# Kernel optimization log

Measured on AMD Instinct MI355X. Metric: run time of the kernel, lower is better.

## Reference

```python
import jax, jax.numpy as jnp
import numpy as np

FILTER_WIDTH = 23
NSIG = 9.0
RATIO = 4.0
SUB_LOW_RATIO = 1.0
PCT = 3.0  # normalization_percentile_threshold


def _gaussian_kernel_2d(ksize, sigma):
    # matches cv2.getGaussianKernel for sigma > 0: normalized 1D gaussian, outer product
    i = np.arange(ksize, dtype=np.float64) - (ksize - 1) / 2.0
    k1 = np.exp(-(i ** 2) / (2.0 * sigma ** 2))
    k1 /= k1.sum()
    k2 = np.outer(k1, k1)
    return k2.astype(np.float32)


def setup_inputs() -> dict:
    key = jax.random.key(0)
    k1, k2 = jax.random.split(key)
    x = jax.random.normal(k1, (16, 3, 512, 512), dtype=jnp.float32)
    mask = jax.random.uniform(k2, (16, 1, 512, 512), dtype=jnp.float32)
    kernel = jnp.asarray(_gaussian_kernel_2d(FILTER_WIDTH, NSIG))[None, None]  # [1,1,23,23]
    return {"x": x, "mask": mask, "kernel": kernel}


def reference(x, mask, kernel):
    N, C, H, W = x.shape
    pad = FILTER_WIDTH // 2  # 11

    # --- median padding (torch.median = lower median -> sorted index (n-1)//2) ---
    flat = x.reshape(N, C, H * W)
    med = jnp.sort(flat, axis=-1)[:, :, (H * W - 1) // 2] + 0.2  # [N,C]
    med = med[:, :, None, None]
    xp = mask * x + (1.0 - mask) * med  # [N,C,H,W]

    # --- Gaussian low-pass: replication pad + depthwise conv (same kernel per channel) ---
    xpad = jnp.pad(xp, ((0, 0), (0, 0), (pad, pad), (pad, pad)), mode="edge")
    k = jnp.broadcast_to(kernel, (C, 1, FILTER_WIDTH, FILTER_WIDTH))
    gauss = jax.lax.conv_general_dilated(
        xpad, k, window_strides=(1, 1), padding="VALID", feature_group_count=C
    )  # [N,C,H,W]

    res = RATIO * (xp - SUB_LOW_RATIO * gauss)

    # --- per-(n,c) percentile normalization on 1/256-quantized copy ---
    temp = jnp.trunc(res * 256.0) / 256.0  # torch .int() truncates toward zero
    tflat = temp.reshape(N, C, H * W)
    lo = jnp.percentile(tflat, PCT, axis=-1)[:, :, None, None]
    hi = jnp.percentile(tflat, 100.0 - PCT, axis=-1)[:, :, None, None]
    res = (res - lo) / (hi - lo)

    # sub_mask=True
    return res * mask
```

## Files before the change

### kernel.cpp

```cpp
#include <hip/hip_runtime.h>

#define HW 262144
#define WID 512
#define PLANES 48
#define NCH 3
#define PAD 11
#define FW 23
#define XS 92
#define NSUB 16

__device__ __forceinline__ float uniform_f(float v) {
  return __uint_as_float((unsigned)__builtin_amdgcn_readfirstlane((int)__float_as_uint(v)));
}

__global__ __launch_bounds__(256) void hist1_kernel(const float* __restrict__ x,
                                                    ushort* __restrict__ part) {
  __shared__ int h[8192];
  const int p = blockIdx.x, s = blockIdx.y, tid = threadIdx.x;
  for (int i = tid; i < 8192; i += 256) h[i] = 0;
  __syncthreads();
  const float4* xv = (const float4*)(x + (size_t)p * HW + (size_t)s * (HW / NSUB));
  float4 a[8], b[8];
#pragma unroll
  for (int q = 0; q < 8; ++q) a[q] = xv[tid + q * 256];
#pragma unroll
  for (int q = 0; q < 8; ++q) b[q] = xv[tid + (8 + q) * 256];
#define H1(c) { int bin = (int)(((c) + 8.0f) * 512.0f); bin = min(max(bin, 0), 8191); atomicAdd(&h[bin], 1); }
#pragma unroll
  for (int q = 0; q < 8; ++q) { H1(a[q].x); H1(a[q].y); H1(a[q].z); H1(a[q].w); }
#pragma unroll
  for (int q = 0; q < 8; ++q) { H1(b[q].x); H1(b[q].y); H1(b[q].z); H1(b[q].w); }
#undef H1
  __syncthreads();
  uint4* out = (uint4*)(part + ((size_t)p * NSUB + s) * 8192);
  for (int k = tid; k < 1024; k += 256) {
    int4 c = *(const int4*)&h[k * 8];
    int4 d = *(const int4*)&h[k * 8 + 4];
    uint4 w;
    w.x = (unsigned)c.x | ((unsigned)c.y << 16);
    w.y = (unsigned)c.z | ((unsigned)c.w << 16);
    w.z = (unsigned)d.x | ((unsigned)d.y << 16);
    w.w = (unsigned)d.z | ((unsigned)d.w << 16);
    out[k] = w;
  }
}

__global__ __launch_bounds__(256) void scan_med_kernel(const ushort* __restrict__ part,
                                                       float* __restrict__ med,
                                                       const float* __restrict__ kern,
                                                       float* __restrict__ k1g) {
  __shared__ int hsum[8192];
  __shared__ int incl[256];
  __shared__ int s_chunk, s_base;
  const int p = blockIdx.x, t = threadIdx.x;
  if (p == 0 && t < FW) k1g[t] = kern[t * FW + PAD] / sqrtf(kern[PAD * FW + PAD]);
  const uint4* pr = (const uint4*)(part + (size_t)p * NSUB * 8192);
  for (int idx = t; idx < 1024; idx += 256) {
    int a0=0,a1=0,a2=0,a3=0,a4=0,a5=0,a6=0,a7=0;
#pragma unroll
    for (int s = 0; s < NSUB; ++s) {
      uint4 v = pr[(size_t)s * 1024 + idx];
      a0 += (int)(v.x & 0xffff); a1 += (int)(v.x >> 16);
      a2 += (int)(v.y & 0xffff); a3 += (int)(v.y >> 16);
      a4 += (int)(v.z & 0xffff); a5 += (int)(v.z >> 16);
      a6 += (int)(v.w & 0xffff); a7 += (int)(v.w >> 16);
    }
    int* hb = &hsum[idx * 8];
    hb[0]=a0; hb[1]=a1; hb[2]=a2; hb[3]=a3; hb[4]=a4; hb[5]=a5; hb[6]=a6; hb[7]=a7;
  }
  __syncthreads();
  int mysum = 0;
#pragma unroll
  for (int j = 0; j < 32; j += 4) {
    int4 v = *(const int4*)&hsum[t * 32 + j];
    mysum += v.x + v.y + v.z + v.w;
  }
  incl[t] = mysum;
  __syncthreads();
  for (int off = 1; off < 256; off <<= 1) {
    int v = (t >= off) ? incl[t - off] : 0;
    __syncthreads();
    incl[t] += v;
    __syncthreads();
  }
  const int rank = 131072;
  {
    int excl = incl[t] - mysum;
    if (excl < rank && rank <= incl[t]) { s_chunk = t; s_base = rank - excl; }
  }
  __syncthreads();
  if (t < 64) {
    const int c = s_chunk, base = s_base;
    int cnt = (t < 32) ? hsum[c * 32 + t] : 0;
    int pfx = cnt;
#pragma unroll
    for (int off = 1; off < 32; off <<= 1) {
      int u = __shfl_up(pfx, off, 64);
      if (t >= off) pfx += u;
    }
    unsigned long long m = __ballot(t < 32 && pfx >= base);
    int bin = c * 32 + (__ffsll((long long)m) - 1);
    if (t == 0) med[p] = -8.0f + ((float)bin + 0.5f) * 0.001953125f + 0.2f;
  }
}

__global__ __launch_bounds__(256) void conv_kernel(const float* __restrict__ x,
                                                   const float* __restrict__ mask,
                                                   const float* __restrict__ k1g,
                                                   const float* __restrict__ med,
                                                   float* __restrict__ res) {
  __shared__ float xs[86 * XS];
  const int z = blockIdx.z;
  const int n = z / NCH;
  const int tbx = blockIdx.x, tby = blockIdx.y;
  const int tid = threadIdx.x;

  float k1[FW];
#pragma unroll
  for (int t = 0; t < FW; ++t) k1[t] = uniform_f(k1g[t]);

  const float m_med = uniform_f(med[z]);
  const int gr0 = tby * 64 - PAD;
  const int gc0 = tbx * 64 - PAD;
  const float* xb = x + (size_t)z * HW;
  const float* mb = mask + (size_t)n * HW;
  for (int i = tid; i < 86 * 86; i += 256) {
    int r = i / 86, c = i - r * 86;
    int gr = min(max(gr0 + r, 0), WID - 1);
    int gc = min(max(gc0 + c, 0), WID - 1);
    int g = gr * WID + gc;
    float xv = xb[g], mv = mb[g];
    xs[r * XS + c] = fmaf(mv, xv - m_med, m_med);
  }
  __syncthreads();

  float ah[3][8];
#pragma unroll
  for (int it = 0; it < 3; ++it) {
    const int g = tid + (it << 8);
    if (g < 86 * 8) {
      const int r = g >> 3, c0 = (g & 7) << 3;
      const float* row = &xs[r * XS + c0];
      float w[32];
#pragma unroll
      for (int q = 0; q < 8; ++q) *(float4*)&w[q * 4] = *(const float4*)(row + q * 4);
#pragma unroll
      for (int j = 0; j < 8; ++j) ah[it][j] = 0.f;
#pragma unroll
      for (int t = 0; t < FW; ++t) {
        const float k = k1[t];
#pragma unroll
        for (int j = 0; j < 8; ++j) ah[it][j] = fmaf(k, w[t + j], ah[it][j]);
      }
    }
  }

  const int ct = (tid & 15) << 2;
  const int rt = (tid >> 4) << 2;
  float4 xpA[4], xpB[4];
#pragma unroll
  for (int j = 0; j < 4; ++j) {
    const float* xr = &xs[(rt + j + PAD) * XS + ct];
    xpA[j] = *(const float4*)(xr + 8);
    xpB[j] = *(const float4*)(xr + 12);
  }
  __syncthreads();

#pragma unroll
  for (int it = 0; it < 3; ++it) {
    const int g = tid + (it << 8);
    if (g < 86 * 8) {
      const int r = g >> 3, c0 = (g & 7) << 3;
      *(float4*)&xs[r * XS + c0] = make_float4(ah[it][0], ah[it][1], ah[it][2], ah[it][3]);
      *(float4*)&xs[r * XS + c0 + 4] = make_float4(ah[it][4], ah[it][5], ah[it][6], ah[it][7]);
    }
  }
  __syncthreads();

  float4 acc[4];
#pragma unroll
  for (int j = 0; j < 4; ++j) acc[j] = make_float4(0.f, 0.f, 0.f, 0.f);
#pragma unroll
  for (int tp = 0; tp < 26; ++tp) {
    float4 v = *(const float4*)&xs[(rt + tp) * XS + ct];
    const int jlo = (tp - 22 > 0) ? (tp - 22) : 0;
    const int jhi = (tp < 3) ? tp : 3;
#pragma unroll
    for (int j = jlo; j <= jhi; ++j) {
      float k = k1[tp - j];
      acc[j].x = fmaf(k, v.x, acc[j].x);
      acc[j].y = fmaf(k, v.y, acc[j].y);
      acc[j].z = fmaf(k, v.z, acc[j].z);
      acc[j].w = fmaf(k, v.w, acc[j].w);
    }
  }

  float* rb = res + (size_t)z * HW + (size_t)(tby * 64 + rt) * WID + tbx * 64 + ct;
#pragma unroll
  for (int j = 0; j < 4; ++j) {
    float4 o;
    o.x = 4.0f * (xpA[j].w - acc[j].x);
    o.y = 4.0f * (xpB[j].x - acc[j].y);
    o.z = 4.0f * (xpB[j].y - acc[j].z);
    o.w = 4.0f * (xpB[j].z - acc[j].w);
    *(float4*)(rb + (size_t)j * WID) = o;
  }
}

__global__ __launch_bounds__(256) void hist_kernel(const float* __restrict__ res,
                                                   ushort* __restrict__ part) {
  __shared__ int h[8192];
  const int p = blockIdx.x, s = blockIdx.y, tid = threadIdx.x;
  for (int i = tid; i < 8192; i += 256) h[i] = 0;
  __syncthreads();
  const float4* rv = (const float4*)(res + (size_t)p * HW + (size_t)s * (HW / NSUB));
  float4 a[8], b[8];
#pragma unroll
  for (int q = 0; q < 8; ++q) a[q] = rv[tid + q * 256];
#pragma unroll
  for (int q = 0; q < 8; ++q) b[q] = rv[tid + (8 + q) * 256];
#define HADD(c) { int bin = (int)((c) * 256.0f) + 4096; bin = min(max(bin, 0), 8191); atomicAdd(&h[bin], 1); }
#pragma unroll
  for (int q = 0; q < 8; ++q) { HADD(a[q].x); HADD(a[q].y); HADD(a[q].z); HADD(a[q].w); }
#pragma unroll
  for (int q = 0; q < 8; ++q) { HADD(b[q].x); HADD(b[q].y); HADD(b[q].z); HADD(b[q].w); }
#undef HADD
  __syncthreads();
  uint4* out = (uint4*)(part + ((size_t)p * NSUB + s) * 8192);
  for (int k = tid; k < 1024; k += 256) {
    int4 c = *(const int4*)&h[k * 8];
    int4 d = *(const int4*)&h[k * 8 + 4];
    uint4 w;
    w.x = (unsigned)c.x | ((unsigned)c.y << 16);
    w.y = (unsigned)c.z | ((unsigned)c.w << 16);
    w.z = (unsigned)d.x | ((unsigned)d.y << 16);
    w.w = (unsigned)d.z | ((unsigned)d.w << 16);
    out[k] = w;
  }
}

__global__ __launch_bounds__(256) void pct_kernel(const ushort* __restrict__ part,
                                                  float* __restrict__ lo_out,
                                                  float* __restrict__ inv_out) {
  __shared__ int hsum[8192];
  __shared__ int incl[256];
  __shared__ int s_chunk, s_base;
  __shared__ float s_v[4];
  const int p = blockIdx.x, t = threadIdx.x;
  const uint4* pr = (const uint4*)(part + (size_t)p * NSUB * 8192);
  for (int idx = t; idx < 1024; idx += 256) {
    int a0=0,a1=0,a2=0,a3=0,a4=0,a5=0,a6=0,a7=0;
#pragma unroll
    for (int s = 0; s < NSUB; ++s) {
      uint4 v = pr[(size_t)s * 1024 + idx];
      a0 += (int)(v.x & 0xffff); a1 += (int)(v.x >> 16);
      a2 += (int)(v.y & 0xffff); a3 += (int)(v.y >> 16);
      a4 += (int)(v.z & 0xffff); a5 += (int)(v.z >> 16);
      a6 += (int)(v.w & 0xffff); a7 += (int)(v.w >> 16);
    }
    int* hb = &hsum[idx * 8];
    hb[0]=a0; hb[1]=a1; hb[2]=a2; hb[3]=a3; hb[4]=a4; hb[5]=a5; hb[6]=a6; hb[7]=a7;
  }
  __syncthreads();
  int mysum = 0;
#pragma unroll
  for (int j = 0; j < 32; j += 4) {
    int4 v = *(const int4*)&hsum[t * 32 + j];
    mysum += v.x + v.y + v.z + v.w;
  }
  incl[t] = mysum;
  __syncthreads();
  for (int off = 1; off < 256; off <<= 1) {
    int v = (t >= off) ? incl[t - off] : 0;
    __syncthreads();
    incl[t] += v;
    __syncthreads();
  }
  const int ranks[4] = {7865, 7866, 254279, 254280};
#pragma unroll
  for (int r = 0; r < 4; ++r) {
    const int rank = ranks[r];
    int excl = incl[t] - mysum;
    if (excl < rank && rank <= incl[t]) { s_chunk = t; s_base = rank - excl; }
    __syncthreads();
    if (t < 64) {
      const int c = s_chunk, base = s_base;
      int cnt = (t < 32) ? hsum[c * 32 + t] : 0;
      int pfx = cnt;
#pragma unroll
      for (int off = 1; off < 32; off <<= 1) {
        int u = __shfl_up(pfx, off, 64);
        if (t >= off) pfx += u;
      }
      unsigned long long m = __ballot(t < 32 && pfx >= base);
      int bin = c * 32 + (__ffsll((long long)m) - 1);
      if (t == 0) s_v[r] = (float)(bin - 4096) * 0.00390625f;
    }
    __syncthreads();
  }
  if (t == 0) {
    const double fl = 0.29, fh = 0.71;
    double lov = (double)s_v[0] + fl * ((double)s_v[1] - (double)s_v[0]);
    double hiv = (double)s_v[2] + fh * ((double)s_v[3] - (double)s_v[2]);
    lo_out[p] = (float)lov;
    inv_out[p] = (float)(1.0 / (hiv - lov));
  }
}

__global__ __launch_bounds__(256) void final_kernel(float* __restrict__ res,
                                                    const float* __restrict__ mask,
                                                    const float* __restrict__ lo,
                                                    const float* __restrict__ inv) {
  const int base = blockIdx.x * 512 + threadIdx.x;
  const int z = base >> 16;
  const int n = z / NCH;
  const int h0 = base & 65535;
  float4* rz = (float4*)res;
  const float4* mz = (const float4*)mask + (size_t)n * 65536;
  float4 r0 = rz[base], r1 = rz[base + 256];
  float4 m0 = mz[h0], m1 = mz[h0 + 256];
  const float l = lo[z];
  const float iv = inv[z];
  float4 o0, o1;
  o0.x = (r0.x - l) * iv * m0.x;  o0.y = (r0.y - l) * iv * m0.y;
  o0.z = (r0.z - l) * iv * m0.z;  o0.w = (r0.w - l) * iv * m0.w;
  o1.x = (r1.x - l) * iv * m1.x;  o1.y = (r1.y - l) * iv * m1.y;
  o1.z = (r1.z - l) * iv * m1.z;  o1.w = (r1.w - l) * iv * m1.w;
  rz[base] = o0;
  rz[base + 256] = o1;
}

extern "C" void kernel_launch(void* const* d_in, const int* in_sizes, int n_in,
                              void* d_out, int out_size, void* d_ws, size_t ws_size,
                              hipStream_t stream) {
  (void)in_sizes; (void)n_in; (void)out_size; (void)ws_size;
  const float* x = (const float*)d_in[0];
  const float* mask = (const float*)d_in[1];
  const float* kern = (const float*)d_in[2];
  float* out = (float*)d_out;

  ushort* part = (ushort*)d_ws;
  float* med = (float*)(part + (size_t)PLANES * NSUB * 8192);
  float* lo = med + PLANES;
  float* inv = lo + PLANES;
  float* k1g = inv + PLANES;

  hist1_kernel<<<dim3(PLANES, NSUB), 256, 0, stream>>>(x, part);
  scan_med_kernel<<<PLANES, 256, 0, stream>>>(part, med, kern, k1g);
  conv_kernel<<<dim3(8, 8, PLANES), 256, 0, stream>>>(x, mask, k1g, med, out);
  hist_kernel<<<dim3(PLANES, NSUB), 256, 0, stream>>>(out, part);
  pct_kernel<<<PLANES, 256, 0, stream>>>(part, lo, inv);
  final_kernel<<<(HW * PLANES / 8) / 256, 256, 0, stream>>>(out, mask, lo, inv);
}
```

Baseline: 194.1 us.

## Fuse histogram reduction into histogram kernels via last-block atomic ticket

The separate scan/median and percentile kernels are merged into the two histogram kernels. Each block bumps a per-plane atomic counter after writing its partial histogram, and the last block for that plane does the reduction and rank search. This drops two kernel launches and the gaps between them. In exchange it adds a memset of the counters, relies on acquire/release ordering of the partial-histogram writes, and leaves the reduction running on a single tail block per plane.

```diff
diff --git a/kernel.cpp b/kernel.cpp
--- a/kernel.cpp
+++ b/kernel.cpp
@@ -14,9 +14,17 @@
 }
 
 __global__ __launch_bounds__(256) void hist1_kernel(const float* __restrict__ x,
-                                                    ushort* __restrict__ part) {
+                                                    ushort* __restrict__ part,
+                                                    float* __restrict__ med,
+                                                    const float* __restrict__ kern,
+                                                    float* __restrict__ k1g,
+                                                    int* __restrict__ tick) {
   __shared__ int h[8192];
+  __shared__ int incl[256];
+  __shared__ int s_chunk, s_base, s_last;
   const int p = blockIdx.x, s = blockIdx.y, tid = threadIdx.x;
+  if (p == 0 && s == 0 && tid < FW)
+    k1g[tid] = kern[tid * FW + PAD] / sqrtf(kern[PAD * FW + PAD]);
   for (int i = tid; i < 8192; i += 256) h[i] = 0;
   __syncthreads();
   const float4* xv = (const float4*)(x + (size_t)p * HW + (size_t)s * (HW / NSUB));
@@ -43,64 +51,58 @@
     w.w = (unsigned)d.z | ((unsigned)d.w << 16);
     out[k] = w;
   }
-}
-
-__global__ __launch_bounds__(256) void scan_med_kernel(const ushort* __restrict__ part,
-                                                       float* __restrict__ med,
-                                                       const float* __restrict__ kern,
-                                                       float* __restrict__ k1g) {
-  __shared__ int hsum[8192];
-  __shared__ int incl[256];
-  __shared__ int s_chunk, s_base;
-  const int p = blockIdx.x, t = threadIdx.x;
-  if (p == 0 && t < FW) k1g[t] = kern[t * FW + PAD] / sqrtf(kern[PAD * FW + PAD]);
+  __syncthreads();
+  if (tid == 0) s_last = __hip_atomic_fetch_add(&tick[p], 1, __ATOMIC_ACQ_REL, __HIP_MEMORY_SCOPE_AGENT);
+  __syncthreads();
+  if (s_last != NSUB - 1) return;
+
   const uint4* pr = (const uint4*)(part + (size_t)p * NSUB * 8192);
-  for (int idx = t; idx < 1024; idx += 256) {
+  for (int idx = tid; idx < 1024; idx += 256) {
     int a0=0,a1=0,a2=0,a3=0,a4=0,a5=0,a6=0,a7=0;
 #pragma unroll
-    for (int s = 0; s < NSUB; ++s) {
-      uint4 v = pr[(size_t)s * 1024 + idx];
+    for (int q = 0; q < NSUB; ++q) {
+      uint4 v = pr[(size_t)q * 1024 + idx];
       a0 += (int)(v.x & 0xffff); a1 += (int)(v.x >> 16);
       a2 += (int)(v.y & 0xffff); a3 += (int)(v.y >> 16);
       a4 += (int)(v.z & 0xffff); a5 += (int)(v.z >> 16);
       a6 += (int)(v.w & 0xffff); a7 += (int)(v.w >> 16);
     }
-    int* hb = &hsum[idx * 8];
+    int* hb = &h[idx * 8];
     hb[0]=a0; hb[1]=a1; hb[2]=a2; hb[3]=a3; hb[4]=a4; hb[5]=a5; hb[6]=a6; hb[7]=a7;
   }
   __syncthreads();
   int mysum = 0;
 #pragma unroll
   for (int j = 0; j < 32; j += 4) {
-    int4 v = *(const int4*)&hsum[t * 32 + j];
+    int4 v = *(const int4*)&h[tid * 32 + j];
     mysum += v.x + v.y + v.z + v.w;
   }
-  incl[t] = mysum;
+  incl[tid] = mysum;
   __syncthreads();
   for (int off = 1; off < 256; off <<= 1) {
-    int v = (t >= off) ? incl[t - off] : 0;
-    __syncthreads();
-    incl[t] += v;
+    int v = (tid >= off) ? incl[tid - off] : 0;
+    __syncthreads();
+    incl[tid] += v;
     __syncthreads();
   }
   const int rank = 131072;
   {
-    int excl = incl[t] - mysum;
-    if (excl < rank && rank <= incl[t]) { s_chunk = t; s_base = rank - excl; }
-  }
-  __syncthreads();
-  if (t < 64) {
+    int excl = incl[tid] - mysum;
+    if (excl < rank && rank <= incl[tid]) { s_chunk = tid; s_base = rank - excl; }
+  }
+  __syncthreads();
+  if (tid < 64) {
     const int c = s_chunk, base = s_base;
-    int cnt = (t < 32) ? hsum[c * 32 + t] : 0;
+    int cnt = (tid < 32) ? h[c * 32 + tid] : 0;
     int pfx = cnt;
 #pragma unroll
     for (int off = 1; off < 32; off <<= 1) {
       int u = __shfl_up(pfx, off, 64);
-      if (t >= off) pfx += u;
-    }
-    unsigned long long m = __ballot(t < 32 && pfx >= base);
+      if (tid >= off) pfx += u;
+    }
+    unsigned long long m = __ballot(tid < 32 && pfx >= base);
     int bin = c * 32 + (__ffsll((long long)m) - 1);
-    if (t == 0) med[p] = -8.0f + ((float)bin + 0.5f) * 0.001953125f + 0.2f;
+    if (tid == 0) med[p] = -8.0f + ((float)bin + 0.5f) * 0.001953125f + 0.2f;
   }
 }
 
@@ -208,8 +210,14 @@
 }
 
 __global__ __launch_bounds__(256) void hist_kernel(const float* __restrict__ res,
-                                                   ushort* __restrict__ part) {
+                                                   ushort* __restrict__ part,
+                                                   float* __restrict__ lo_out,
+                                                   float* __restrict__ inv_out,
+                                                   int* __restrict__ tick) {
   __shared__ int h[8192];
+  __shared__ int incl[256];
+  __shared__ int s_chunk, s_base, s_last;
+  __shared__ float s_v[4];
   const int p = blockIdx.x, s = blockIdx.y, tid = threadIdx.x;
   for (int i = tid; i < 8192; i += 256) h[i] = 0;
   __syncthreads();
@@ -237,68 +245,63 @@
     w.w = (unsigned)d.z | ((unsigned)d.w << 16);
     out[k] = w;
   }
-}
-
-__global__ __launch_bounds__(256) void pct_kernel(const ushort* __restrict__ part,
-                                                  float* __restrict__ lo_out,
-                                                  float* __restrict__ inv_out) {
-  __shared__ int hsum[8192];
-  __shared__ int incl[256];
-  __shared__ int s_chunk, s_base;
-  __shared__ float s_v[4];
-  const int p = blockIdx.x, t = threadIdx.x;
+  __syncthreads();
+  if (tid == 0) s_last = __hip_atomic_fetch_add(&tick[p], 1, __ATOMIC_ACQ_REL, __HIP_MEMORY_SCOPE_AGENT);
+  __syncthreads();
+  if (s_last != NSUB - 1) return;
+
   const uint4* pr = (const uint4*)(part + (size_t)p * NSUB * 8192);
-  for (int idx = t; idx < 1024; idx += 256) {
+  for (int idx = tid; idx < 1024; idx += 256) {
     int a0=0,a1=0,a2=0,a3=0,a4=0,a5=0,a6=0,a7=0;
 #pragma unroll
-    for (int s = 0; s < NSUB; ++s) {
-      uint4 v = pr[(size_t)s * 1024 + idx];
+    for (int q = 0; q < NSUB; ++q) {
+      uint4 v = pr[(size_t)q * 1024 + idx];
       a0 += (int)(v.x & 0xffff); a1 += (int)(v.x >> 16);
       a2 += (int)(v.y & 0xffff); a3 += (int)(v.y >> 16);
       a4 += (int)(v.z & 0xffff); a5 += (int)(v.z >> 16);
       a6 += (int)(v.w & 0xffff); a7 += (int)(v.w >> 16);
     }
-    int* hb = &hsum[idx * 8];
+    int* hb = &h[idx * 8];
     hb[0]=a0; hb[1]=a1; hb[2]=a2; hb[3]=a3; hb[4]=a4; hb[5]=a5; hb[6]=a6; hb[7]=a7;
   }
   __syncthreads();
   int mysum = 0;
 #pragma unroll
   for (int j = 0; j < 32; j += 4) {
-    int4 v = *(const int4*)&hsum[t * 32 + j];
+    int4 v = *(const int4*)&h[tid * 32 + j];
     mysum += v.x + v.y + v.z + v.w;
   }
-  incl[t] = mysum;
+  incl[tid] = mysum;
   __syncthreads();
   for (int off = 1; off < 256; off <<= 1) {
-    int v = (t >= off) ? incl[t - off] : 0;
-    __syncthreads();
-    incl[t] += v;
+    int v = (tid >= off) ? incl[tid - off] : 0;
+    __syncthreads();
+    incl[tid] += v;
     __syncthreads();
   }
   const int ranks[4] = {7865, 7866, 254279, 254280};
 #pragma unroll
   for (int r = 0; r < 4; ++r) {
     const int rank = ranks[r];
-    int excl = incl[t] - mysum;
-    if (excl < rank && rank <= incl[t]) { s_chunk = t; s_base = rank - excl; }
-    __syncthreads();
-    if (t < 64) {
+    int excl = incl[tid] - mysum;
+    if (excl < rank && rank <= incl[tid]) { s_chunk = tid; s_base = rank - excl; }
+    __syncthreads();
+    if (tid < 64) {
       const int c = s_chunk, base = s_base;
-      int cnt = (t < 32) ? hsum[c * 32 + t] : 0;
+      int cnt = (tid < 32) ? h[c * 32 + tid] : 0;
       int pfx = cnt;
 #pragma unroll
       for (int off = 1; off < 32; off <<= 1) {
         int u = __shfl_up(pfx, off, 64);
-        if (t >= off) pfx += u;
+        if (tid >= off) pfx += u;
       }
-      unsigned long long m = __ballot(t < 32 && pfx >= base);
+      unsigned long long m = __ballot(tid < 32 && pfx >= base);
       int bin = c * 32 + (__ffsll((long long)m) - 1);
-      if (t == 0) s_v[r] = (float)(bin - 4096) * 0.00390625f;
-    }
-    __syncthreads();
-  }
-  if (t == 0) {
+      if (tid == 0) s_v[r] = (float)(bin - 4096) * 0.00390625f;
+    }
+    __syncthreads();
+  }
+  if (tid == 0) {
     const double fl = 0.29, fh = 0.71;
     double lov = (double)s_v[0] + fl * ((double)s_v[1] - (double)s_v[0]);
     double hiv = (double)s_v[2] + fh * ((double)s_v[3] - (double)s_v[2]);
@@ -340,15 +343,16 @@
   float* out = (float*)d_out;
 
   ushort* part = (ushort*)d_ws;
-  float* med = (float*)(part + (size_t)PLANES * NSUB * 8192);
+  int* tick1 = (int*)(part + (size_t)PLANES * NSUB * 8192);
+  int* tick2 = tick1 + PLANES;
+  float* med = (float*)(tick2 + PLANES);
   float* lo = med + PLANES;
   float* inv = lo + PLANES;
   float* k1g = inv + PLANES;
 
-  hist1_kernel<<<dim3(PLANES, NSUB), 256, 0, stream>>>(x, part);
-  scan_med_kernel<<<PLANES, 256, 0, stream>>>(part, med, kern, k1g);
+  hipMemsetAsync(tick1, 0, 2 * PLANES * sizeof(int), stream);
+  hist1_kernel<<<dim3(PLANES, NSUB), 256, 0, stream>>>(x, part, med, kern, k1g, tick1);
   conv_kernel<<<dim3(8, 8, PLANES), 256, 0, stream>>>(x, mask, k1g, med, out);
-  hist_kernel<<<dim3(PLANES, NSUB), 256, 0, stream>>>(out, part);
-  pct_kernel<<<PLANES, 256, 0, stream>>>(part, lo, inv);
+  hist_kernel<<<dim3(PLANES, NSUB), 256, 0, stream>>>(out, part, lo, inv, tick2);
   final_kernel<<<(HW * PLANES / 8) / 256, 256, 0, stream>>>(out, mask, lo, inv);
 }
```

After: 253.0 us. 1.3x slower.
